# Performance work log

Hardware: AMD Instinct MI355X
Metric: run time of the kernel (lower is better)

Reference implementation:

```python
import jax, jax.numpy as jnp
import numpy as np

NUM_HEADS = 4

def setup_inputs() -> dict:
    key = jax.random.key(0)
    k1, k2, k3, k4 = jax.random.split(key, 4)
    B, N, D = 8, 768, 2048
    x = jax.random.normal(k1, (B, N, D), dtype=jnp.float32)
    s = 1.0 / np.sqrt(N)
    W_qk = jax.random.normal(k2, (N, N), dtype=jnp.float32) * s
    W_v = jax.random.normal(k3, (N, N), dtype=jnp.float32) * s
    W_out = jax.random.normal(k4, (N, N), dtype=jnp.float32) * s
    return {"x": x, "W_qk": W_qk, "W_v": W_v, "W_out": W_out}

def reference(x, W_qk, W_v, W_out):
    B, N, D = x.shape
    H = NUM_HEADS
    n = N // H
    y = jnp.swapaxes(x, 1, 2)                    # (B, D, N): attention over channels D
    qk = y @ W_qk.T                              # (B, D, N)
    v = y @ W_v.T                                # (B, D, N)
    # to heads: (B, D, N) -> (B, H, D, n)
    qk = jnp.swapaxes(qk.reshape(B, D, H, n), 1, 2)
    v = jnp.swapaxes(v.reshape(B, D, H, n), 1, 2)
    dot = jnp.einsum('bhdn,bhen->bhde', qk, qk)  # (B, H, D, D)
    q2 = jnp.sum(qk * qk, axis=-1)               # (B, H, D)
    # negative squared Euclidean distance logits: 2*q.k - ||q||^2 - ||k||^2
    logits = 2.0 * dot - q2[..., :, None] - q2[..., None, :]
    attn = jax.nn.softmax(logits, axis=-1)
    w = jnp.einsum('bhde,bhen->bhdn', attn, v)   # (B, H, D, n)
    # from heads: (B, H, D, n) -> (B, D, N)
    w = jnp.swapaxes(w, 1, 2).reshape(B, D, N)
    out = w @ W_out.T                            # (B, D, N)
    return jnp.swapaxes(out, 1, 2)               # (B, N, D)
```

## Files before the change

kernel.cpp:

```cpp
#include <hip/hip_runtime.h>
#include <stdint.h>

#define B_  8
#define N_  768
#define D_  2048
#define H_  4
#define HN  192

#define QROW 200
#define VROW 72
#define KTILE_B 25600
#define VTILE_B 27648

#define LOG2E 1.4426950408889634f
#define C2    2.8853901617f

typedef unsigned short u16;
typedef float    f32x4 __attribute__((ext_vector_type(4)));
typedef __bf16   bf16x8 __attribute__((ext_vector_type(8)));
typedef __bf16   bf16x4 __attribute__((ext_vector_type(4)));
typedef uint32_t u32x4 __attribute__((ext_vector_type(4)));
typedef uint32_t u32x2 __attribute__((ext_vector_type(2)));

__device__ __forceinline__ u16 f2bf(float f) {
  return __builtin_bit_cast(u16, (__bf16)f);
}

typedef const __attribute__((address_space(1))) void* gas_ptr;
typedef __attribute__((address_space(3))) void* las_ptr;
__device__ __forceinline__ void gld16(const void* g, void* l) {
  __builtin_amdgcn_global_load_lds((gas_ptr)g, (las_ptr)l, 16, 0, 0);
}

__global__ __launch_bounds__(256) void prep(const float* __restrict__ x,
                                            const float* __restrict__ Wqk,
                                            const float* __restrict__ Wv,
                                            const float* __restrict__ Wout,
                                            u16* __restrict__ xt,
                                            u16* __restrict__ oqk,
                                            u16* __restrict__ ov,
                                            u16* __restrict__ oout,
                                            float* __restrict__ q2) {
  __shared__ float tile[64][65];
  const int bid = blockIdx.x;
  const int t   = threadIdx.x;
  if (bid < 3072) {
    const int d0 = (bid & 31) * 64;
    const int n0 = ((bid >> 5) % 12) * 64;
    const int b  = (bid >> 5) / 12;
    const int col = t & 63;
    const int rb  = (t >> 6) * 16;
    const float* src = x + ((size_t)b * N_ + n0) * D_ + d0;
    #pragma unroll
    for (int i = 0; i < 16; i++)
      tile[rb + i][col] = src[(size_t)(rb + i) * D_ + col];
    __syncthreads();
    u16* dst = xt + ((size_t)b * D_ + d0) * N_ + n0;
    #pragma unroll
    for (int i = 0; i < 16; i++)
      dst[(size_t)(rb + i) * N_ + col] = f2bf(tile[col][rb + i]);
  } else if (bid < 4800) {
    const int r   = bid - 3072;
    const int mat = r / 576;
    const float* src = (mat == 0) ? Wqk : ((mat == 1) ? Wv : Wout);
    u16*         dst = (mat == 0) ? oqk : ((mat == 1) ? ov : oout);
    const int i = ((r % 576) * 256 + t) * 4;
    f32x4 v = *(const f32x4*)(src + i);
    bf16x4 tmp;
    #pragma unroll
    for (int j = 0; j < 4; j++) tmp[j] = (__bf16)v[j];
    *(bf16x4*)(dst + i) = tmp;
  } else {
    const f32x4 fz = {0.f, 0.f, 0.f, 0.f};
    const int i = ((bid - 4800) * 256 + t) * 4;
    *(f32x4*)(q2 + i) = fz;
  }
}

__global__ __launch_bounds__(256, 2) void qkv_gemm(const u16* __restrict__ xt,
                                                   const u16* __restrict__ wqk,
                                                   const u16* __restrict__ wv,
                                                   u16* __restrict__ qkb,
                                                   u16* __restrict__ vtb,
                                                   float* __restrict__ q2) {
  const int b     = blockIdx.z;
  const int dtile = blockIdx.x;
  const int d0    = dtile * 128;
  const int j0    = blockIdx.y * 128;
  const int tid  = threadIdx.x;
  const int wave = tid >> 6, lane = tid & 63;
  const int l15  = lane & 15, quad = lane >> 4;
  const int wm = wave >> 1, wn = wave & 1;

  __shared__ u16 At[128 * 64];
  __shared__ u16 Bq[128 * 64];
  __shared__ u16 Bv[128 * 64];

  const f32x4 fz = {0.f, 0.f, 0.f, 0.f};
  f32x4 accq[4][4];
  f32x4 accv[4][4];
  #pragma unroll
  for (int i = 0; i < 4; i++)
    #pragma unroll
    for (int j = 0; j < 4; j++) { accq[i][j] = fz; accv[i][j] = fz; }

  const int srow  = tid >> 3;
  const int sbyte = (tid & 7) * 16;
  const u16* ax = xt  + ((size_t)b * D_ + d0 + srow) * N_;
  const u16* bq = wqk + (size_t)(j0 + srow) * N_;
  const u16* bv = wv  + (size_t)(j0 + srow) * N_;

  for (int k0 = 0; k0 < N_; k0 += 64) {
    __syncthreads();
    #pragma unroll
    for (int c = 0; c < 4; c++) {
      gld16((const char*)(ax + (size_t)c * 32 * N_ + k0) + sbyte,
            (char*)At + c * 4096 + tid * 16);
      gld16((const char*)(bq + (size_t)c * 32 * N_ + k0) + sbyte,
            (char*)Bq + c * 4096 + tid * 16);
      gld16((const char*)(bv + (size_t)c * 32 * N_ + k0) + sbyte,
            (char*)Bv + c * 4096 + tid * 16);
    }
    __syncthreads();

    #pragma unroll
    for (int kk = 0; kk < 2; kk++) {
      bf16x8 Af[4];
      #pragma unroll
      for (int mi = 0; mi < 4; mi++)
        Af[mi] = *(const bf16x8*)&At[(wm * 64 + mi * 16 + l15) * 64 + kk * 32 + quad * 8];
      #pragma unroll
      for (int ni = 0; ni < 4; ni++) {
        bf16x8 Bqf = *(const bf16x8*)&Bq[(wn * 64 + ni * 16 + l15) * 64 + kk * 32 + quad * 8];
        bf16x8 Bvf = *(const bf16x8*)&Bv[(wn * 64 + ni * 16 + l15) * 64 + kk * 32 + quad * 8];
        #pragma unroll
        for (int mi = 0; mi < 4; mi++) {
          accq[ni][mi] = __builtin_amdgcn_mfma_f32_16x16x32_bf16(Bqf, Af[mi], accq[ni][mi], 0, 0, 0);
          accv[mi][ni] = __builtin_amdgcn_mfma_f32_16x16x32_bf16(Af[mi], Bvf, accv[mi][ni], 0, 0, 0);
        }
      }
    }
  }

  const int h_w  = (j0 + wn * 64) / HN;
  const int jn_w = (j0 + wn * 64) % HN;
  const size_t bh = (size_t)b * H_ + h_w;

  #pragma unroll
  for (int md = 0; md < 4; md++) {
    float s = 0.f;
    #pragma unroll
    for (int nj = 0; nj < 4; nj++)
      #pragma unroll
      for (int r = 0; r < 4; r++) { float v = accq[nj][md][r]; s += v * v; }
    s += __shfl_xor(s, 16, 64);
    s += __shfl_xor(s, 32, 64);
    if (quad == 0)
      atomicAdd(&q2[bh * D_ + d0 + wm * 64 + md * 16 + l15], s * LOG2E);
  }

  u16* qtbase = qkb + bh * (size_t)(D_ * QROW);
  #pragma unroll
  for (int md = 0; md < 4; md++) {
    const size_t dro = (size_t)(d0 + wm * 64 + md * 16 + l15) * QROW;
    #pragma unroll
    for (int nj = 0; nj < 4; nj++) {
      bf16x4 tmp;
      #pragma unroll
      for (int r = 0; r < 4; r++) tmp[r] = (__bf16)accq[nj][md][r];
      *(bf16x4*)(qtbase + dro + jn_w + nj * 16 + quad * 4) = tmp;
    }
  }

  const int etile = dtile * 2 + wm;
  u16* vtbase = vtb + bh * (size_t)(32 * HN * VROW) + (size_t)etile * (HN * VROW);
  #pragma unroll
  for (int ni = 0; ni < 4; ni++) {
    const size_t jro = (size_t)(jn_w + ni * 16 + l15) * VROW;
    #pragma unroll
    for (int mi = 0; mi < 4; mi++) {
      bf16x4 tmp;
      #pragma unroll
      for (int r = 0; r < 4; r++) tmp[r] = (__bf16)accv[mi][ni][r];
      *(bf16x4*)(vtbase + jro + mi * 16 + quad * 4) = tmp;
    }
  }
}

__global__ __launch_bounds__(256, 2) void attn_kernel(const u16* __restrict__ qkb,
                                                      const u16* __restrict__ vtb,
                                                      const float* __restrict__ q2,
                                                      u16* __restrict__ wbuf) {
  const int bid  = blockIdx.x;
  const int bh   = (bid & 7) * 4 + (bid >> 7);
  const int dblk = (bid >> 3) & 15;
  const int b = bh >> 2, h = bh & 3;
  const int tid  = threadIdx.x;
  const int wave = tid >> 6, lane = tid & 63;
  const int l15  = lane & 15, quad = lane >> 4;

  __shared__ u16 Klds[64 * QROW];
  __shared__ u16 Vlds[HN * VROW];
  __shared__ u16 Plds[4][32][VROW];

  const u16* kg = qkb + (size_t)bh * (D_ * QROW);
  const u16* vg = vtb + (size_t)bh * (32 * HN * VROW);
  const float* q2g = q2 + (size_t)bh * D_;

  bf16x8 Qf[2][6];
  {
    const u16* qrow = kg + (size_t)(dblk * 128 + wave * 32 + l15) * QROW + quad * 8;
    #pragma unroll
    for (int nt = 0; nt < 2; nt++)
      #pragma unroll
      for (int f = 0; f < 6; f++)
        Qf[nt][f] = *(const bf16x8*)(qrow + (size_t)nt * 16 * QROW + f * 32);
  }
  float cd[2];
  cd[0] = q2g[dblk * 128 + wave * 32 + l15];
  cd[1] = q2g[dblk * 128 + wave * 32 + 16 + l15];

  bf16x8 OnesF;
  #pragma unroll
  for (int j = 0; j < 8; j++) OnesF[j] = (__bf16)1.0f;

  const f32x4 fz = {0.f, 0.f, 0.f, 0.f};
  f32x4 O[2][12];
  f32x4 Or[2];
  #pragma unroll
  for (int mt = 0; mt < 2; mt++) {
    Or[mt] = fz;
    #pragma unroll
    for (int c = 0; c < 12; c++) O[mt][c] = fz;
  }

  for (int t = 0; t < 32; t++) {
    __syncthreads();
    {
      const char* ks = (const char*)kg + (size_t)t * KTILE_B;
      char* kd = (char*)Klds;
      for (int c = wave; c < 25; c += 4)
        gld16(ks + c * 1024 + lane * 16, kd + c * 1024 + lane * 16);
      const char* vs = (const char*)vg + (size_t)t * VTILE_B;
      char* vd = (char*)Vlds;
      for (int c = wave; c < 27; c += 4)
        gld16(vs + c * 1024 + lane * 16, vd + c * 1024 + lane * 16);
    }
    __syncthreads();

    #pragma unroll
    for (int et = 0; et < 4; et++) {
      bf16x8 Kf[6];
      #pragma unroll
      for (int f = 0; f < 6; f++)
        Kf[f] = *(const bf16x8*)&Klds[(et * 16 + l15) * QROW + f * 32 + quad * 8];
      f32x4 S0 = fz, S1 = fz;
      __builtin_amdgcn_s_setprio(1);
      #pragma unroll
      for (int f = 0; f < 6; f++) {
        S0 = __builtin_amdgcn_mfma_f32_16x16x32_bf16(Kf[f], Qf[0][f], S0, 0, 0, 0);
        S1 = __builtin_amdgcn_mfma_f32_16x16x32_bf16(Kf[f], Qf[1][f], S1, 0, 0, 0);
      }
      __builtin_amdgcn_s_setprio(0);
      const f32x4 ce = *(const f32x4*)&q2g[t * 64 + et * 16 + quad * 4];
      bf16x4 pb0, pb1;
      #pragma unroll
      for (int r = 0; r < 4; r++) {
        float p0 = __builtin_amdgcn_exp2f(__builtin_fmaf(S0[r], C2, -(ce[r] + cd[0])));
        float p1 = __builtin_amdgcn_exp2f(__builtin_fmaf(S1[r], C2, -(ce[r] + cd[1])));
        pb0[r] = (__bf16)p0;
        pb1[r] = (__bf16)p1;
      }
      *(bf16x4*)&Plds[wave][l15][et * 16 + quad * 4]      = pb0;
      *(bf16x4*)&Plds[wave][16 + l15][et * 16 + quad * 4] = pb1;
    }

    #pragma unroll
    for (int kk = 0; kk < 2; kk++) {
      bf16x8 Pf0 = *(const bf16x8*)&Plds[wave][l15][kk * 32 + quad * 8];
      bf16x8 Pf1 = *(const bf16x8*)&Plds[wave][16 + l15][kk * 32 + quad * 8];
      __builtin_amdgcn_s_setprio(1);
      #pragma unroll
      for (int c = 0; c < 12; c++) {
        bf16x8 Vf = *(const bf16x8*)&Vlds[(c * 16 + l15) * VROW + kk * 32 + quad * 8];
        O[0][c] = __builtin_amdgcn_mfma_f32_16x16x32_bf16(Pf0, Vf, O[0][c], 0, 0, 0);
        O[1][c] = __builtin_amdgcn_mfma_f32_16x16x32_bf16(Pf1, Vf, O[1][c], 0, 0, 0);
      }
      Or[0] = __builtin_amdgcn_mfma_f32_16x16x32_bf16(Pf0, OnesF, Or[0], 0, 0, 0);
      Or[1] = __builtin_amdgcn_mfma_f32_16x16x32_bf16(Pf1, OnesF, Or[1], 0, 0, 0);
      __builtin_amdgcn_s_setprio(0);
    }
  }

  #pragma unroll
  for (int mt = 0; mt < 2; mt++)
    #pragma unroll
    for (int r = 0; r < 4; r++) {
      const float inv = __builtin_amdgcn_rcpf(Or[mt][r]);
      const int d = dblk * 128 + wave * 32 + mt * 16 + quad * 4 + r;
      u16* wrow = wbuf + ((size_t)b * D_ + d) * N_ + h * HN;
      #pragma unroll
      for (int c = 0; c < 12; c++)
        wrow[c * 16 + l15] = f2bf(O[mt][c][r] * inv);
    }
}

__global__ __launch_bounds__(256, 2) void out_gemm(const u16* __restrict__ wbuf,
                                                   const u16* __restrict__ wout,
                                                   float* __restrict__ outp) {
  const int b  = blockIdx.z;
  const int d0 = blockIdx.x * 128;
  const int i0 = blockIdx.y * 128;
  const int tid  = threadIdx.x;
  const int wave = tid >> 6, lane = tid & 63;
  const int l15  = lane & 15, quad = lane >> 4;
  const int wm = wave >> 1, wn = wave & 1;

  __shared__ u16 At[128 * 64];
  __shared__ u16 Bt[128 * 64];

  const f32x4 fz = {0.f, 0.f, 0.f, 0.f};
  f32x4 acc[4][4];
  #pragma unroll
  for (int i = 0; i < 4; i++)
    #pragma unroll
    for (int j = 0; j < 4; j++) acc[i][j] = fz;

  const int srow  = tid >> 3;
  const int sbyte = (tid & 7) * 16;
  const u16* ax = wbuf + ((size_t)b * D_ + d0 + srow) * N_;
  const u16* bw = wout + (size_t)(i0 + srow) * N_;

  for (int k0 = 0; k0 < N_; k0 += 64) {
    __syncthreads();
    #pragma unroll
    for (int c = 0; c < 4; c++) {
      gld16((const char*)(ax + (size_t)c * 32 * N_ + k0) + sbyte,
            (char*)At + c * 4096 + tid * 16);
      gld16((const char*)(bw + (size_t)c * 32 * N_ + k0) + sbyte,
            (char*)Bt + c * 4096 + tid * 16);
    }
    __syncthreads();

    #pragma unroll
    for (int kk = 0; kk < 2; kk++) {
      bf16x8 Af[4];
      #pragma unroll
      for (int mi = 0; mi < 4; mi++)
        Af[mi] = *(const bf16x8*)&At[(wm * 64 + mi * 16 + l15) * 64 + kk * 32 + quad * 8];
      #pragma unroll
      for (int ni = 0; ni < 4; ni++) {
        bf16x8 Bf = *(const bf16x8*)&Bt[(wn * 64 + ni * 16 + l15) * 64 + kk * 32 + quad * 8];
        #pragma unroll
        for (int mi = 0; mi < 4; mi++)
          acc[mi][ni] = __builtin_amdgcn_mfma_f32_16x16x32_bf16(Af[mi], Bf, acc[mi][ni], 0, 0, 0);
      }
    }
  }

  #pragma unroll
  for (int ni = 0; ni < 4; ni++) {
    float* orow = outp + ((size_t)b * N_ + i0 + wn * 64 + ni * 16 + l15) * D_
                + d0 + wm * 64 + quad * 4;
    #pragma unroll
    for (int mi = 0; mi < 4; mi++)
      *(f32x4*)(orow + mi * 16) = acc[mi][ni];
  }
}

extern "C" void kernel_launch(void* const* d_in, const int* in_sizes, int n_in,
                              void* d_out, int out_size, void* d_ws, size_t ws_size,
                              hipStream_t stream) {
  (void)in_sizes; (void)n_in; (void)out_size; (void)ws_size;
  const float* x    = (const float*)d_in[0];
  const float* Wqk  = (const float*)d_in[1];
  const float* Wv   = (const float*)d_in[2];
  const float* Wout = (const float*)d_in[3];
  float* outp = (float*)d_out;

  char* ws = (char*)d_ws;
  size_t off = 0;
  u16* xt   = (u16*)(ws + off); off += (size_t)B_ * D_ * N_ * 2;
  u16* qkb  = (u16*)(ws + off); off += (size_t)B_ * H_ * D_ * QROW * 2;
  u16* vtb  = (u16*)(ws + off); off += (size_t)B_ * H_ * 32 * HN * VROW * 2;
  float* q2 = (float*)(ws + off); off += (size_t)B_ * H_ * D_ * 4;
  u16* wqk_bf  = (u16*)(ws + off); off += (size_t)N_ * N_ * 2;
  u16* wv_bf   = (u16*)(ws + off); off += (size_t)N_ * N_ * 2;
  u16* wout_bf = (u16*)(ws + off); off += (size_t)N_ * N_ * 2;
  u16* wbuf = xt;

  prep<<<dim3(4864), 256, 0, stream>>>(x, Wqk, Wv, Wout, xt, wqk_bf, wv_bf, wout_bf, q2);
  qkv_gemm<<<dim3(D_ / 128, N_ / 128, B_), 256, 0, stream>>>(xt, wqk_bf, wv_bf, qkb, vtb, q2);
  attn_kernel<<<dim3((D_ / 128) * B_ * H_), 256, 0, stream>>>(qkb, vtb, q2, wbuf);
  out_gemm<<<dim3(D_ / 128, N_ / 128, B_), 256, 0, stream>>>(wbuf, wout_bf, outp);
}
```

Before: 293.3 us.

## Double-buffer LDS tiles in QKV and output GEMM kernels

Both GEMM kernels now use two LDS buffers. The next K-tile's global-to-LDS loads are issued before computing on the current tile, and each iteration needs only one barrier instead of two. This is meant to hide global load latency behind the MFMA work. The QKV kernel halves its K-tile to 32 so its LDS footprint stays the same, at the cost of twice as many iterations and barriers. The output GEMM doubles its LDS use to 64KB per block, which may limit how many blocks fit on a CU.

```diff
diff --git a/kernel.cpp b/kernel.cpp
--- a/kernel.cpp
+++ b/kernel.cpp
@@ -92,9 +92,9 @@
   const int l15  = lane & 15, quad = lane >> 4;
   const int wm = wave >> 1, wn = wave & 1;
 
-  __shared__ u16 At[128 * 64];
-  __shared__ u16 Bq[128 * 64];
-  __shared__ u16 Bv[128 * 64];
+  __shared__ u16 At[2][128 * 32];
+  __shared__ u16 Bq[2][128 * 32];
+  __shared__ u16 Bv[2][128 * 32];
 
   const f32x4 fz = {0.f, 0.f, 0.f, 0.f};
   f32x4 accq[4][4];
@@ -104,40 +104,44 @@
     #pragma unroll
     for (int j = 0; j < 4; j++) { accq[i][j] = fz; accv[i][j] = fz; }
 
-  const int srow  = tid >> 3;
-  const int sbyte = (tid & 7) * 16;
+  const int srow  = tid >> 2;
+  const int sbyte = (tid & 3) * 16;
   const u16* ax = xt  + ((size_t)b * D_ + d0 + srow) * N_;
   const u16* bq = wqk + (size_t)(j0 + srow) * N_;
   const u16* bv = wv  + (size_t)(j0 + srow) * N_;
 
-  for (int k0 = 0; k0 < N_; k0 += 64) {
+  #define QSTAGE(BUF, K0)                                                   \
+    { _Pragma("unroll")                                                     \
+      for (int c = 0; c < 2; c++) {                                         \
+        gld16((const char*)(ax + (size_t)c * 64 * N_ + (K0)) + sbyte,       \
+              (char*)At[BUF] + c * 4096 + tid * 16);                        \
+        gld16((const char*)(bq + (size_t)c * 64 * N_ + (K0)) + sbyte,       \
+              (char*)Bq[BUF] + c * 4096 + tid * 16);                        \
+        gld16((const char*)(bv + (size_t)c * 64 * N_ + (K0)) + sbyte,       \
+              (char*)Bv[BUF] + c * 4096 + tid * 16);                        \
+      } }
+
+  QSTAGE(0, 0);
+
+  for (int t = 0; t < 24; t++) {
     __syncthreads();
-    #pragma unroll
-    for (int c = 0; c < 4; c++) {
-      gld16((const char*)(ax + (size_t)c * 32 * N_ + k0) + sbyte,
-            (char*)At + c * 4096 + tid * 16);
-      gld16((const char*)(bq + (size_t)c * 32 * N_ + k0) + sbyte,
-            (char*)Bq + c * 4096 + tid * 16);
-      gld16((const char*)(bv + (size_t)c * 32 * N_ + k0) + sbyte,
-            (char*)Bv + c * 4096 + tid * 16);
-    }
-    __syncthreads();
-
-    #pragma unroll
-    for (int kk = 0; kk < 2; kk++) {
-      bf16x8 Af[4];
-      #pragma unroll
-      for (int mi = 0; mi < 4; mi++)
-        Af[mi] = *(const bf16x8*)&At[(wm * 64 + mi * 16 + l15) * 64 + kk * 32 + quad * 8];
-      #pragma unroll
-      for (int ni = 0; ni < 4; ni++) {
-        bf16x8 Bqf = *(const bf16x8*)&Bq[(wn * 64 + ni * 16 + l15) * 64 + kk * 32 + quad * 8];
-        bf16x8 Bvf = *(const bf16x8*)&Bv[(wn * 64 + ni * 16 + l15) * 64 + kk * 32 + quad * 8];
-        #pragma unroll
-        for (int mi = 0; mi < 4; mi++) {
-          accq[ni][mi] = __builtin_amdgcn_mfma_f32_16x16x32_bf16(Bqf, Af[mi], accq[ni][mi], 0, 0, 0);
-          accv[mi][ni] = __builtin_amdgcn_mfma_f32_16x16x32_bf16(Af[mi], Bvf, accv[mi][ni], 0, 0, 0);
-        }
+    if (t < 23) QSTAGE((t + 1) & 1, (t + 1) * 32);
+    const u16* at = At[t & 1];
+    const u16* bqt = Bq[t & 1];
+    const u16* bvt = Bv[t & 1];
+
+    bf16x8 Af[4];
+    #pragma unroll
+    for (int mi = 0; mi < 4; mi++)
+      Af[mi] = *(const bf16x8*)&at[(wm * 64 + mi * 16 + l15) * 32 + quad * 8];
+    #pragma unroll
+    for (int ni = 0; ni < 4; ni++) {
+      bf16x8 Bqf = *(const bf16x8*)&bqt[(wn * 64 + ni * 16 + l15) * 32 + quad * 8];
+      bf16x8 Bvf = *(const bf16x8*)&bvt[(wn * 64 + ni * 16 + l15) * 32 + quad * 8];
+      #pragma unroll
+      for (int mi = 0; mi < 4; mi++) {
+        accq[ni][mi] = __builtin_amdgcn_mfma_f32_16x16x32_bf16(Bqf, Af[mi], accq[ni][mi], 0, 0, 0);
+        accv[mi][ni] = __builtin_amdgcn_mfma_f32_16x16x32_bf16(Af[mi], Bvf, accv[mi][ni], 0, 0, 0);
       }
     }
   }
@@ -316,8 +320,8 @@
   const int l15  = lane & 15, quad = lane >> 4;
   const int wm = wave >> 1, wn = wave & 1;
 
-  __shared__ u16 At[128 * 64];
-  __shared__ u16 Bt[128 * 64];
+  __shared__ u16 At[2][128 * 64];
+  __shared__ u16 Bt[2][128 * 64];
 
   const f32x4 fz = {0.f, 0.f, 0.f, 0.f};
   f32x4 acc[4][4];
@@ -331,26 +335,32 @@
   const u16* ax = wbuf + ((size_t)b * D_ + d0 + srow) * N_;
   const u16* bw = wout + (size_t)(i0 + srow) * N_;
 
-  for (int k0 = 0; k0 < N_; k0 += 64) {
+  #define OSTAGE(BUF, K0)                                                   \
+    { _Pragma("unroll")                                                     \
+      for (int c = 0; c < 4; c++) {                                         \
+        gld16((const char*)(ax + (size_t)c * 32 * N_ + (K0)) + sbyte,       \
+              (char*)At[BUF] + c * 4096 + tid * 16);                        \
+        gld16((const char*)(bw + (size_t)c * 32 * N_ + (K0)) + sbyte,       \
+              (char*)Bt[BUF] + c * 4096 + tid * 16);                        \
+      } }
+
+  OSTAGE(0, 0);
+
+  for (int t = 0; t < 12; t++) {
     __syncthreads();
-    #pragma unroll
-    for (int c = 0; c < 4; c++) {
-      gld16((const char*)(ax + (size_t)c * 32 * N_ + k0) + sbyte,
-            (char*)At + c * 4096 + tid * 16);
-      gld16((const char*)(bw + (size_t)c * 32 * N_ + k0) + sbyte,
-            (char*)Bt + c * 4096 + tid * 16);
-    }
-    __syncthreads();
+    if (t < 11) OSTAGE((t + 1) & 1, (t + 1) * 64);
+    const u16* at = At[t & 1];
+    const u16* bt = Bt[t & 1];
 
     #pragma unroll
     for (int kk = 0; kk < 2; kk++) {
       bf16x8 Af[4];
       #pragma unroll
       for (int mi = 0; mi < 4; mi++)
-        Af[mi] = *(const bf16x8*)&At[(wm * 64 + mi * 16 + l15) * 64 + kk * 32 + quad * 8];
+        Af[mi] = *(const bf16x8*)&at[(wm * 64 + mi * 16 + l15) * 64 + kk * 32 + quad * 8];
       #pragma unroll
       for (int ni = 0; ni < 4; ni++) {
-        bf16x8 Bf = *(const bf16x8*)&Bt[(wn * 64 + ni * 16 + l15) * 64 + kk * 32 + quad * 8];
+        bf16x8 Bf = *(const bf16x8*)&bt[(wn * 64 + ni * 16 + l15) * 64 + kk * 32 + quad * 8];
         #pragma unroll
         for (int mi = 0; mi < 4; mi++)
           acc[mi][ni] = __builtin_amdgcn_mfma_f32_16x16x32_bf16(Af[mi], Bf, acc[mi][ni], 0, 0, 0);
```

Measured after the change: 299.0 us. About the same (+1.9%).

## Split fused QKV GEMM, enlarge tiles to 256x192, double-buffer LDS loads

Applied to the files above, without the earlier changes.

Splits the fused QK/V projection GEMM into two separate kernels. The QKV and output GEMMs now use 512-thread blocks with 256x192 tiles (one head per block), K steps of 32, and double-buffered LDS staging that prefetches the next K slice while the current one is computed. This is meant to raise reuse per loaded element, drop one of the two barriers per K step, and overlap global loads with MFMA work. In exchange, x is now read twice, once per projection kernel, and the grids shrink to 256 and 192 blocks, which may underfill the 256 CUs.

```diff
diff --git a/kernel.cpp b/kernel.cpp
--- a/kernel.cpp
+++ b/kernel.cpp
@@ -77,112 +77,165 @@
   }
 }
 
-__global__ __launch_bounds__(256, 2) void qkv_gemm(const u16* __restrict__ xt,
-                                                   const u16* __restrict__ wqk,
-                                                   const u16* __restrict__ wv,
-                                                   u16* __restrict__ qkb,
-                                                   u16* __restrict__ vtb,
-                                                   float* __restrict__ q2) {
-  const int b     = blockIdx.z;
-  const int dtile = blockIdx.x;
-  const int d0    = dtile * 128;
-  const int j0    = blockIdx.y * 128;
+
+__global__ __launch_bounds__(512, 2) void qk_gemm(const u16* __restrict__ xt,
+                                                  const u16* __restrict__ wqk,
+                                                  u16* __restrict__ qkb,
+                                                  float* __restrict__ q2) {
+  const int b  = blockIdx.z;
+  const int d0 = blockIdx.x * 256;
+  const int h  = blockIdx.y;
+  const int j0 = h * HN;
   const int tid  = threadIdx.x;
   const int wave = tid >> 6, lane = tid & 63;
   const int l15  = lane & 15, quad = lane >> 4;
-  const int wm = wave >> 1, wn = wave & 1;
-
-  __shared__ u16 At[128 * 64];
-  __shared__ u16 Bq[128 * 64];
-  __shared__ u16 Bv[128 * 64];
+  const int wm = wave >> 2, wn = wave & 3;
+
+  __shared__ u16 At[2][256 * 32];
+  __shared__ u16 Bt[2][192 * 32];
 
   const f32x4 fz = {0.f, 0.f, 0.f, 0.f};
-  f32x4 accq[4][4];
-  f32x4 accv[4][4];
-  #pragma unroll
-  for (int i = 0; i < 4; i++)
-    #pragma unroll
-    for (int j = 0; j < 4; j++) { accq[i][j] = fz; accv[i][j] = fz; }
-
-  const int srow  = tid >> 3;
-  const int sbyte = (tid & 7) * 16;
+  f32x4 acc[3][8];
+  #pragma unroll
+  for (int i = 0; i < 3; i++)
+    #pragma unroll
+    for (int j = 0; j < 8; j++) acc[i][j] = fz;
+
+  const int srow  = tid >> 2;
+  const int sbyte = (tid & 3) * 16;
   const u16* ax = xt  + ((size_t)b * D_ + d0 + srow) * N_;
   const u16* bq = wqk + (size_t)(j0 + srow) * N_;
-  const u16* bv = wv  + (size_t)(j0 + srow) * N_;
-
-  for (int k0 = 0; k0 < N_; k0 += 64) {
-    __syncthreads();
-    #pragma unroll
-    for (int c = 0; c < 4; c++) {
-      gld16((const char*)(ax + (size_t)c * 32 * N_ + k0) + sbyte,
-            (char*)At + c * 4096 + tid * 16);
-      gld16((const char*)(bq + (size_t)c * 32 * N_ + k0) + sbyte,
-            (char*)Bq + c * 4096 + tid * 16);
-      gld16((const char*)(bv + (size_t)c * 32 * N_ + k0) + sbyte,
-            (char*)Bv + c * 4096 + tid * 16);
-    }
-    __syncthreads();
-
-    #pragma unroll
-    for (int kk = 0; kk < 2; kk++) {
-      bf16x8 Af[4];
-      #pragma unroll
-      for (int mi = 0; mi < 4; mi++)
-        Af[mi] = *(const bf16x8*)&At[(wm * 64 + mi * 16 + l15) * 64 + kk * 32 + quad * 8];
-      #pragma unroll
-      for (int ni = 0; ni < 4; ni++) {
-        bf16x8 Bqf = *(const bf16x8*)&Bq[(wn * 64 + ni * 16 + l15) * 64 + kk * 32 + quad * 8];
-        bf16x8 Bvf = *(const bf16x8*)&Bv[(wn * 64 + ni * 16 + l15) * 64 + kk * 32 + quad * 8];
-        #pragma unroll
-        for (int mi = 0; mi < 4; mi++) {
-          accq[ni][mi] = __builtin_amdgcn_mfma_f32_16x16x32_bf16(Bqf, Af[mi], accq[ni][mi], 0, 0, 0);
-          accv[mi][ni] = __builtin_amdgcn_mfma_f32_16x16x32_bf16(Af[mi], Bvf, accv[mi][ni], 0, 0, 0);
-        }
-      }
-    }
-  }
-
-  const int h_w  = (j0 + wn * 64) / HN;
-  const int jn_w = (j0 + wn * 64) % HN;
-  const size_t bh = (size_t)b * H_ + h_w;
-
-  #pragma unroll
-  for (int md = 0; md < 4; md++) {
+
+  #define KSTG(BUF, K0)                                                       \
+    { gld16((const char*)(ax + (K0)) + sbyte, (char*)At[BUF] + tid * 16);     \
+      gld16((const char*)(ax + (size_t)128 * N_ + (K0)) + sbyte,              \
+            (char*)At[BUF] + 8192 + tid * 16);                                \
+      gld16((const char*)(bq + (K0)) + sbyte, (char*)Bt[BUF] + tid * 16);     \
+      if (tid < 256)                                                          \
+        gld16((const char*)(bq + (size_t)128 * N_ + (K0)) + sbyte,            \
+              (char*)Bt[BUF] + 8192 + tid * 16); }
+
+  KSTG(0, 0);
+
+  for (int t = 0; t < 24; t++) {
+    __syncthreads();
+    if (t < 23) KSTG((t + 1) & 1, (t + 1) * 32);
+    const u16* at = At[t & 1];
+    const u16* bt = Bt[t & 1];
+
+    bf16x8 Af[8];
+    #pragma unroll
+    for (int mi = 0; mi < 8; mi++)
+      Af[mi] = *(const bf16x8*)&at[(wm * 128 + mi * 16 + l15) * 32 + quad * 8];
+    #pragma unroll
+    for (int nj = 0; nj < 3; nj++) {
+      bf16x8 Bf = *(const bf16x8*)&bt[(wn * 48 + nj * 16 + l15) * 32 + quad * 8];
+      #pragma unroll
+      for (int mi = 0; mi < 8; mi++)
+        acc[nj][mi] = __builtin_amdgcn_mfma_f32_16x16x32_bf16(Bf, Af[mi], acc[nj][mi], 0, 0, 0);
+    }
+  }
+
+  const size_t bh = (size_t)b * H_ + h;
+
+  #pragma unroll
+  for (int md = 0; md < 8; md++) {
     float s = 0.f;
     #pragma unroll
-    for (int nj = 0; nj < 4; nj++)
-      #pragma unroll
-      for (int r = 0; r < 4; r++) { float v = accq[nj][md][r]; s += v * v; }
+    for (int nj = 0; nj < 3; nj++)
+      #pragma unroll
+      for (int r = 0; r < 4; r++) { float v = acc[nj][md][r]; s += v * v; }
     s += __shfl_xor(s, 16, 64);
     s += __shfl_xor(s, 32, 64);
     if (quad == 0)
-      atomicAdd(&q2[bh * D_ + d0 + wm * 64 + md * 16 + l15], s * LOG2E);
+      atomicAdd(&q2[bh * D_ + d0 + wm * 128 + md * 16 + l15], s * LOG2E);
   }
 
   u16* qtbase = qkb + bh * (size_t)(D_ * QROW);
   #pragma unroll
-  for (int md = 0; md < 4; md++) {
-    const size_t dro = (size_t)(d0 + wm * 64 + md * 16 + l15) * QROW;
-    #pragma unroll
-    for (int nj = 0; nj < 4; nj++) {
+  for (int md = 0; md < 8; md++) {
+    const size_t dro = (size_t)(d0 + wm * 128 + md * 16 + l15) * QROW;
+    #pragma unroll
+    for (int nj = 0; nj < 3; nj++) {
       bf16x4 tmp;
       #pragma unroll
-      for (int r = 0; r < 4; r++) tmp[r] = (__bf16)accq[nj][md][r];
-      *(bf16x4*)(qtbase + dro + jn_w + nj * 16 + quad * 4) = tmp;
-    }
-  }
-
-  const int etile = dtile * 2 + wm;
-  u16* vtbase = vtb + bh * (size_t)(32 * HN * VROW) + (size_t)etile * (HN * VROW);
-  #pragma unroll
-  for (int ni = 0; ni < 4; ni++) {
-    const size_t jro = (size_t)(jn_w + ni * 16 + l15) * VROW;
-    #pragma unroll
-    for (int mi = 0; mi < 4; mi++) {
+      for (int r = 0; r < 4; r++) tmp[r] = (__bf16)acc[nj][md][r];
+      *(bf16x4*)(qtbase + dro + wn * 48 + nj * 16 + quad * 4) = tmp;
+    }
+  }
+}
+
+__global__ __launch_bounds__(512, 2) void v_gemm(const u16* __restrict__ xt,
+                                                 const u16* __restrict__ wv,
+                                                 u16* __restrict__ vtb) {
+  const int b  = blockIdx.z;
+  const int dtile = blockIdx.x;
+  const int d0 = dtile * 256;
+  const int h  = blockIdx.y;
+  const int j0 = h * HN;
+  const int tid  = threadIdx.x;
+  const int wave = tid >> 6, lane = tid & 63;
+  const int l15  = lane & 15, quad = lane >> 4;
+  const int wm = wave >> 2, wn = wave & 3;
+
+  __shared__ u16 At[2][256 * 32];
+  __shared__ u16 Bt[2][192 * 32];
+
+  const f32x4 fz = {0.f, 0.f, 0.f, 0.f};
+  f32x4 acc[8][3];
+  #pragma unroll
+  for (int i = 0; i < 8; i++)
+    #pragma unroll
+    for (int j = 0; j < 3; j++) acc[i][j] = fz;
+
+  const int srow  = tid >> 2;
+  const int sbyte = (tid & 3) * 16;
+  const u16* ax = xt + ((size_t)b * D_ + d0 + srow) * N_;
+  const u16* bv = wv + (size_t)(j0 + srow) * N_;
+
+  #define VSTG(BUF, K0)                                                       \
+    { gld16((const char*)(ax + (K0)) + sbyte, (char*)At[BUF] + tid * 16);     \
+      gld16((const char*)(ax + (size_t)128 * N_ + (K0)) + sbyte,              \
+            (char*)At[BUF] + 8192 + tid * 16);                                \
+      gld16((const char*)(bv + (K0)) + sbyte, (char*)Bt[BUF] + tid * 16);     \
+      if (tid < 256)                                                          \
+        gld16((const char*)(bv + (size_t)128 * N_ + (K0)) + sbyte,            \
+              (char*)Bt[BUF] + 8192 + tid * 16); }
+
+  VSTG(0, 0);
+
+  for (int t = 0; t < 24; t++) {
+    __syncthreads();
+    if (t < 23) VSTG((t + 1) & 1, (t + 1) * 32);
+    const u16* at = At[t & 1];
+    const u16* bt = Bt[t & 1];
+
+    bf16x8 Af[8];
+    #pragma unroll
+    for (int mi = 0; mi < 8; mi++)
+      Af[mi] = *(const bf16x8*)&at[(wm * 128 + mi * 16 + l15) * 32 + quad * 8];
+    #pragma unroll
+    for (int ni = 0; ni < 3; ni++) {
+      bf16x8 Bf = *(const bf16x8*)&bt[(wn * 48 + ni * 16 + l15) * 32 + quad * 8];
+      #pragma unroll
+      for (int mi = 0; mi < 8; mi++)
+        acc[mi][ni] = __builtin_amdgcn_mfma_f32_16x16x32_bf16(Af[mi], Bf, acc[mi][ni], 0, 0, 0);
+    }
+  }
+
+  const size_t bh = (size_t)b * H_ + h;
+  u16* vtbase = vtb + bh * (size_t)(32 * HN * VROW);
+  #pragma unroll
+  for (int mi = 0; mi < 8; mi++) {
+    const int etile = dtile * 4 + wm * 2 + (mi >> 2);
+    const int el    = (mi & 3) * 16 + quad * 4;
+    u16* base = vtbase + (size_t)etile * (HN * VROW);
+    #pragma unroll
+    for (int ni = 0; ni < 3; ni++) {
       bf16x4 tmp;
       #pragma unroll
-      for (int r = 0; r < 4; r++) tmp[r] = (__bf16)accv[mi][ni][r];
-      *(bf16x4*)(vtbase + jro + mi * 16 + quad * 4) = tmp;
+      for (int r = 0; r < 4; r++) tmp[r] = (__bf16)acc[mi][ni][r];
+      *(bf16x4*)(base + (size_t)(wn * 48 + ni * 16 + l15) * VROW + el) = tmp;
     }
   }
 }
@@ -305,65 +358,68 @@
     }
 }
 
-__global__ __launch_bounds__(256, 2) void out_gemm(const u16* __restrict__ wbuf,
+__global__ __launch_bounds__(512, 2) void out_gemm(const u16* __restrict__ wbuf,
                                                    const u16* __restrict__ wout,
                                                    float* __restrict__ outp) {
   const int b  = blockIdx.z;
-  const int d0 = blockIdx.x * 128;
-  const int i0 = blockIdx.y * 128;
+  const int d0 = blockIdx.x * 256;
+  const int i0 = blockIdx.y * 192;
   const int tid  = threadIdx.x;
   const int wave = tid >> 6, lane = tid & 63;
   const int l15  = lane & 15, quad = lane >> 4;
-  const int wm = wave >> 1, wn = wave & 1;
-
-  __shared__ u16 At[128 * 64];
-  __shared__ u16 Bt[128 * 64];
+  const int wm = wave >> 2, wn = wave & 3;
+
+  __shared__ u16 At[2][256 * 32];
+  __shared__ u16 Bt[2][192 * 32];
 
   const f32x4 fz = {0.f, 0.f, 0.f, 0.f};
-  f32x4 acc[4][4];
-  #pragma unroll
-  for (int i = 0; i < 4; i++)
-    #pragma unroll
-    for (int j = 0; j < 4; j++) acc[i][j] = fz;
-
-  const int srow  = tid >> 3;
-  const int sbyte = (tid & 7) * 16;
+  f32x4 acc[8][3];
+  #pragma unroll
+  for (int i = 0; i < 8; i++)
+    #pragma unroll
+    for (int j = 0; j < 3; j++) acc[i][j] = fz;
+
+  const int srow  = tid >> 2;
+  const int sbyte = (tid & 3) * 16;
   const u16* ax = wbuf + ((size_t)b * D_ + d0 + srow) * N_;
   const u16* bw = wout + (size_t)(i0 + srow) * N_;
 
-  for (int k0 = 0; k0 < N_; k0 += 64) {
-    __syncthreads();
-    #pragma unroll
-    for (int c = 0; c < 4; c++) {
-      gld16((const char*)(ax + (size_t)c * 32 * N_ + k0) + sbyte,
-            (char*)At + c * 4096 + tid * 16);
-      gld16((const char*)(bw + (size_t)c * 32 * N_ + k0) + sbyte,
-            (char*)Bt + c * 4096 + tid * 16);
-    }
-    __syncthreads();
-
-    #pragma unroll
-    for (int kk = 0; kk < 2; kk++) {
-      bf16x8 Af[4];
-      #pragma unroll
-      for (int mi = 0; mi < 4; mi++)
-        Af[mi] = *(const bf16x8*)&At[(wm * 64 + mi * 16 + l15) * 64 + kk * 32 + quad * 8];
-      #pragma unroll
-      for (int ni = 0; ni < 4; ni++) {
-        bf16x8 Bf = *(const bf16x8*)&Bt[(wn * 64 + ni * 16 + l15) * 64 + kk * 32 + quad * 8];
-        #pragma unroll
-        for (int mi = 0; mi < 4; mi++)
-          acc[mi][ni] = __builtin_amdgcn_mfma_f32_16x16x32_bf16(Af[mi], Bf, acc[mi][ni], 0, 0, 0);
-      }
-    }
-  }
-
-  #pragma unroll
-  for (int ni = 0; ni < 4; ni++) {
-    float* orow = outp + ((size_t)b * N_ + i0 + wn * 64 + ni * 16 + l15) * D_
-                + d0 + wm * 64 + quad * 4;
-    #pragma unroll
-    for (int mi = 0; mi < 4; mi++)
+  #define OSTG(BUF, K0)                                                       \
+    { gld16((const char*)(ax + (K0)) + sbyte, (char*)At[BUF] + tid * 16);     \
+      gld16((const char*)(ax + (size_t)128 * N_ + (K0)) + sbyte,              \
+            (char*)At[BUF] + 8192 + tid * 16);                                \
+      gld16((const char*)(bw + (K0)) + sbyte, (char*)Bt[BUF] + tid * 16);     \
+      if (tid < 256)                                                          \
+        gld16((const char*)(bw + (size_t)128 * N_ + (K0)) + sbyte,            \
+              (char*)Bt[BUF] + 8192 + tid * 16); }
+
+  OSTG(0, 0);
+
+  for (int t = 0; t < 24; t++) {
+    __syncthreads();
+    if (t < 23) OSTG((t + 1) & 1, (t + 1) * 32);
+    const u16* at = At[t & 1];
+    const u16* bt = Bt[t & 1];
+
+    bf16x8 Af[8];
+    #pragma unroll
+    for (int mi = 0; mi < 8; mi++)
+      Af[mi] = *(const bf16x8*)&at[(wm * 128 + mi * 16 + l15) * 32 + quad * 8];
+    #pragma unroll
+    for (int ni = 0; ni < 3; ni++) {
+      bf16x8 Bf = *(const bf16x8*)&bt[(wn * 48 + ni * 16 + l15) * 32 + quad * 8];
+      #pragma unroll
+      for (int mi = 0; mi < 8; mi++)
+        acc[mi][ni] = __builtin_amdgcn_mfma_f32_16x16x32_bf16(Af[mi], Bf, acc[mi][ni], 0, 0, 0);
+    }
+  }
+
+  #pragma unroll
+  for (int ni = 0; ni < 3; ni++) {
+    float* orow = outp + ((size_t)b * N_ + i0 + wn * 48 + ni * 16 + l15) * D_
+                + d0 + wm * 128 + quad * 4;
+    #pragma unroll
+    for (int mi = 0; mi < 8; mi++)
       *(f32x4*)(orow + mi * 16) = acc[mi][ni];
   }
 }
@@ -390,7 +446,8 @@
   u16* wbuf = xt;
 
   prep<<<dim3(4864), 256, 0, stream>>>(x, Wqk, Wv, Wout, xt, wqk_bf, wv_bf, wout_bf, q2);
-  qkv_gemm<<<dim3(D_ / 128, N_ / 128, B_), 256, 0, stream>>>(xt, wqk_bf, wv_bf, qkb, vtb, q2);
+  qk_gemm<<<dim3(D_ / 256, H_, B_), 512, 0, stream>>>(xt, wqk_bf, qkb, q2);
+  v_gemm<<<dim3(D_ / 256, H_, B_), 512, 0, stream>>>(xt, wv_bf, vtb);
   attn_kernel<<<dim3((D_ / 128) * B_ * H_), 256, 0, stream>>>(qkb, vtb, q2, wbuf);
-  out_gemm<<<dim3(D_ / 128, N_ / 128, B_), 256, 0, stream>>>(wbuf, wout_bf, outp);
-}
+  out_gemm<<<dim3(D_ / 256, N_ / 192, B_), 512, 0, stream>>>(wbuf, wout_bf, outp);
+}
```

Result: slower. 301.8 us (+2.9%).

## Feed softmax probabilities directly from registers via 16x16x16 MFMA, drop P LDS round-trip

Applied to the files above, without the earlier changes.

The attention kernel now uses the 16x16x16 bf16 MFMA when it is available, so the probability tile held in the QK^T accumulator layout can serve directly as the A operand of the PV product. This removes the per-wave Plds shared-memory store and reload and frees that LDS. The cost is twice as many MFMA instructions with half the K depth for the PV and row-sum products, which may have lower throughput than the 16x16x32 variant on this hardware.

```diff
diff --git a/kernel.cpp b/kernel.cpp
--- a/kernel.cpp
+++ b/kernel.cpp
@@ -19,8 +19,19 @@
 typedef float    f32x4 __attribute__((ext_vector_type(4)));
 typedef __bf16   bf16x8 __attribute__((ext_vector_type(8)));
 typedef __bf16   bf16x4 __attribute__((ext_vector_type(4)));
+typedef short    s16x4  __attribute__((ext_vector_type(4)));
 typedef uint32_t u32x4 __attribute__((ext_vector_type(4)));
 typedef uint32_t u32x2 __attribute__((ext_vector_type(2)));
+
+#if __has_builtin(__builtin_amdgcn_mfma_f32_16x16x16bf16_1k)
+#define HAVE_MFMA16 1
+__device__ __forceinline__ f32x4 mfma16(bf16x4 a, bf16x4 b, f32x4 c) {
+  return __builtin_amdgcn_mfma_f32_16x16x16bf16_1k(
+      __builtin_bit_cast(s16x4, a), __builtin_bit_cast(s16x4, b), c, 0, 0, 0);
+}
+#else
+#define HAVE_MFMA16 0
+#endif
 
 __device__ __forceinline__ u16 f2bf(float f) {
   return __builtin_bit_cast(u16, (__bf16)f);
@@ -201,7 +212,9 @@
 
   __shared__ u16 Klds[64 * QROW];
   __shared__ u16 Vlds[HN * VROW];
+#if !HAVE_MFMA16
   __shared__ u16 Plds[4][32][VROW];
+#endif
 
   const u16* kg = qkb + (size_t)bh * (D_ * QROW);
   const u16* vg = vtb + (size_t)bh * (32 * HN * VROW);
@@ -220,9 +233,15 @@
   cd[0] = q2g[dblk * 128 + wave * 32 + l15];
   cd[1] = q2g[dblk * 128 + wave * 32 + 16 + l15];
 
+#if HAVE_MFMA16
+  bf16x4 Ones4;
+  #pragma unroll
+  for (int j = 0; j < 4; j++) Ones4[j] = (__bf16)1.0f;
+#else
   bf16x8 OnesF;
   #pragma unroll
   for (int j = 0; j < 8; j++) OnesF[j] = (__bf16)1.0f;
+#endif
 
   const f32x4 fz = {0.f, 0.f, 0.f, 0.f};
   f32x4 O[2][12];
@@ -248,6 +267,42 @@
     }
     __syncthreads();
 
+#if HAVE_MFMA16
+    #pragma unroll
+    for (int et = 0; et < 4; et++) {
+      bf16x8 Kf[6];
+      #pragma unroll
+      for (int f = 0; f < 6; f++)
+        Kf[f] = *(const bf16x8*)&Klds[(et * 16 + l15) * QROW + f * 32 + quad * 8];
+      f32x4 S0 = fz, S1 = fz;
+      __builtin_amdgcn_s_setprio(1);
+      #pragma unroll
+      for (int f = 0; f < 6; f++) {
+        S0 = __builtin_amdgcn_mfma_f32_16x16x32_bf16(Kf[f], Qf[0][f], S0, 0, 0, 0);
+        S1 = __builtin_amdgcn_mfma_f32_16x16x32_bf16(Kf[f], Qf[1][f], S1, 0, 0, 0);
+      }
+      __builtin_amdgcn_s_setprio(0);
+      const f32x4 ce = *(const f32x4*)&q2g[t * 64 + et * 16 + quad * 4];
+      bf16x4 pa0, pa1;
+      #pragma unroll
+      for (int r = 0; r < 4; r++) {
+        float p0 = __builtin_amdgcn_exp2f(__builtin_fmaf(S0[r], C2, -(ce[r] + cd[0])));
+        float p1 = __builtin_amdgcn_exp2f(__builtin_fmaf(S1[r], C2, -(ce[r] + cd[1])));
+        pa0[r] = (__bf16)p0;
+        pa1[r] = (__bf16)p1;
+      }
+      __builtin_amdgcn_s_setprio(1);
+      #pragma unroll
+      for (int c = 0; c < 12; c++) {
+        bf16x4 Vf = *(const bf16x4*)&Vlds[(c * 16 + l15) * VROW + et * 16 + quad * 4];
+        O[0][c] = mfma16(pa0, Vf, O[0][c]);
+        O[1][c] = mfma16(pa1, Vf, O[1][c]);
+      }
+      Or[0] = mfma16(pa0, Ones4, Or[0]);
+      Or[1] = mfma16(pa1, Ones4, Or[1]);
+      __builtin_amdgcn_s_setprio(0);
+    }
+#else
     #pragma unroll
     for (int et = 0; et < 4; et++) {
       bf16x8 Kf[6];
@@ -274,7 +329,6 @@
       *(bf16x4*)&Plds[wave][l15][et * 16 + quad * 4]      = pb0;
       *(bf16x4*)&Plds[wave][16 + l15][et * 16 + quad * 4] = pb1;
     }
-
     #pragma unroll
     for (int kk = 0; kk < 2; kk++) {
       bf16x8 Pf0 = *(const bf16x8*)&Plds[wave][l15][kk * 32 + quad * 8];
@@ -290,6 +344,7 @@
       Or[1] = __builtin_amdgcn_mfma_f32_16x16x32_bf16(Pf1, OnesF, Or[1], 0, 0, 0);
       __builtin_amdgcn_s_setprio(0);
     }
+#endif
   }
 
   #pragma unroll
```

Result: slower. 318.3 us (+8.5%).
